# Kernel tuning notes

Measured on AMD Instinct MI355X. Metric: run time of the kernel, lower is better.

The kernel has to match this reference:

```python
import jax, jax.numpy as jnp
import numpy as np

BOUND = 25      # max decode steps
SOS = 1         # start-of-sequence token index
TEMP = 1.0      # temperature


def setup_inputs() -> dict:
    key = jax.random.key(0)
    ks = jax.random.split(key, 10)
    V, E, H, A, S = 50257, 1024, 1024, 1024, 2048
    return {
        "hidden": jax.random.normal(ks[0], (1, 1, H), dtype=jnp.float32),
        "embeddings": jax.random.normal(ks[1], (1, S, A), dtype=jnp.float32),
        "emb_table": jax.random.normal(ks[2], (V, E), dtype=jnp.float32) * 0.02,
        "W_ih": jax.random.normal(ks[3], (3 * H, E), dtype=jnp.float32) / np.sqrt(E).astype(np.float32),
        "W_hh": jax.random.normal(ks[4], (3 * H, H), dtype=jnp.float32) / np.sqrt(H).astype(np.float32),
        "b_ih": jnp.zeros((3 * H,), jnp.float32),
        "b_hh": jnp.zeros((3 * H,), jnp.float32),
        "W_e": jax.random.normal(ks[5], (A, A), dtype=jnp.float32) / np.sqrt(A).astype(np.float32),
        "W_q": jax.random.normal(ks[6], (A, H), dtype=jnp.float32) / np.sqrt(H).astype(np.float32),
        "b_a": jnp.zeros((A,), jnp.float32),
        "v_a": jax.random.normal(ks[7], (A,), dtype=jnp.float32) / np.sqrt(A).astype(np.float32),
        "W_out": jax.random.normal(ks[8], (V, H + A), dtype=jnp.float32) / np.sqrt(H + A).astype(np.float32),
        "b_out": jnp.zeros((V,), jnp.float32),
    }


def reference(hidden, embeddings, emb_table, W_ih, W_hh, b_ih, b_hh,
              W_e, W_q, b_a, v_a, W_out, b_out):
    """Greedy (top-1) autoregressive decode: per-step GRU + additive attention +
    vocab projection + softmax/argmax, for BOUND steps (EOS break replaced by
    fixed-length scan; faithful math per step, eval mode so dropout = identity).
    Returns (words [BOUND] int32, attention weights [1, BOUND, S])."""
    e = embeddings[0]                         # (S, A) encoder states
    eproj = e @ W_e.T + b_a                   # (S, A) precomputed key projection

    def step(carry, _):
        h, word = carry                       # h: (1, H), word: () int32
        x = emb_table[word][None, :]          # (1, E) input embedding
        # torch nn.GRU single-layer cell
        gi = x @ W_ih.T + b_ih                # (1, 3H)
        gh = h @ W_hh.T + b_hh                # (1, 3H)
        i_r, i_z, i_n = jnp.split(gi, 3, axis=-1)
        h_r, h_z, h_n = jnp.split(gh, 3, axis=-1)
        r = jax.nn.sigmoid(i_r + h_r)
        z = jax.nn.sigmoid(i_z + h_z)
        n = jnp.tanh(i_n + r * h_n)
        h = (1.0 - z) * n + z * h             # (1, H)
        # additive attention over encoder states (query broadcast over S)
        s = jnp.tanh(eproj + h @ W_q.T) @ v_a # (S,)
        w = jax.nn.softmax(s)                 # (S,) attention weights
        ctx = w @ e                           # (A,) context vector
        merge = jnp.concatenate([h[0], ctx])  # (H + A,) = cat([hidden[-1], attn])
        logits = (merge @ W_out.T + b_out) / TEMP   # (V,)
        word = jnp.argmax(logits).astype(jnp.int32) # top-1 sample
        return (h, word), (word, w)

    h0 = hidden[0]                            # last layer of encoder hidden (1, H)
    _, (words, weights) = jax.lax.scan(step, (h0, jnp.int32(SOS)), None, length=BOUND)
    return words, weights[None]               # (BOUND,), (1, BOUND, S)
```

## Files before the change

kernel.cpp:

```cpp
#include <hip/hip_runtime.h>
#include <cmath>

#define HSZ   1024
#define SSZ   2048
#define VSZ   50257
#define BOUND 25
#define SOS   1

__global__ __launch_bounds__(256) void init_kernel(const float* __restrict__ hidden,
                                                   float* __restrict__ h0,
                                                   int* __restrict__ wordp) {
    int i = blockIdx.x * 256 + threadIdx.x;
    if (i < HSZ) h0[i] = hidden[i];
    if (i == 0) *wordp = SOS;
}

#define BM 64
#define BN 64
#define BK 16
__global__ __launch_bounds__(256) void eproj_kernel(const float* __restrict__ e,
                                                    const float* __restrict__ We,
                                                    const float* __restrict__ b_a,
                                                    float* __restrict__ eproj) {
    __shared__ __align__(16) float As[BK][BM];
    __shared__ __align__(16) float Bs[BK][BN];
    const int tid = threadIdx.x;
    const int tx = tid & 15, ty = tid >> 4;
    const int arow0 = blockIdx.x * BM;
    const int brow0 = blockIdx.y * BN;
    const int lr = tid >> 2;
    const int lc = (tid & 3) * 4;

    float acc[4][4] = {};
    for (int k0 = 0; k0 < HSZ; k0 += BK) {
        float4 av = *(const float4*)&e [(size_t)(arow0 + lr) * HSZ + k0 + lc];
        float4 bv = *(const float4*)&We[(size_t)(brow0 + lr) * HSZ + k0 + lc];
        As[lc + 0][lr] = av.x; As[lc + 1][lr] = av.y;
        As[lc + 2][lr] = av.z; As[lc + 3][lr] = av.w;
        Bs[lc + 0][lr] = bv.x; Bs[lc + 1][lr] = bv.y;
        Bs[lc + 2][lr] = bv.z; Bs[lc + 3][lr] = bv.w;
        __syncthreads();
#pragma unroll
        for (int kk = 0; kk < BK; kk++) {
            float4 a4 = *(const float4*)&As[kk][ty * 4];
            float4 b4 = *(const float4*)&Bs[kk][tx * 4];
            float a[4] = {a4.x, a4.y, a4.z, a4.w};
            float b[4] = {b4.x, b4.y, b4.z, b4.w};
#pragma unroll
            for (int i = 0; i < 4; i++)
#pragma unroll
                for (int j = 0; j < 4; j++) acc[i][j] += a[i] * b[j];
        }
        __syncthreads();
    }
#pragma unroll
    for (int i = 0; i < 4; i++) {
        int s = arow0 + ty * 4 + i;
#pragma unroll
        for (int j = 0; j < 4; j++) {
            int a = brow0 + tx * 4 + j;
            eproj[(size_t)s * HSZ + a] = acc[i][j] + b_a[a];
        }
    }
}

__global__ __launch_bounds__(256) void gru_kernel(const float* __restrict__ emb_table,
                                                  const float* __restrict__ W_ih,
                                                  const float* __restrict__ W_hh,
                                                  const float* __restrict__ b_ih,
                                                  const float* __restrict__ b_hh,
                                                  const float* __restrict__ h_old,
                                                  const int* __restrict__ wordp,
                                                  float* __restrict__ h_new) {
    const int j = blockIdx.x;
    const int t = threadIdx.x;
    const int word = *wordp;
    const float* __restrict__ x = emb_table + (size_t)word * HSZ;

    float acc[6] = {0.f, 0.f, 0.f, 0.f, 0.f, 0.f};
    for (int c = t; c < HSZ; c += 256) {
        float xv = x[c], hv = h_old[c];
#pragma unroll
        for (int g = 0; g < 3; g++) {
            acc[g]     += W_ih[(size_t)(g * HSZ + j) * HSZ + c] * xv;
            acc[3 + g] += W_hh[(size_t)(g * HSZ + j) * HSZ + c] * hv;
        }
    }
    __shared__ float red[256];
    __shared__ float res[6];
    for (int g = 0; g < 6; g++) {
        red[t] = acc[g];
        __syncthreads();
        for (int s2 = 128; s2 > 0; s2 >>= 1) {
            if (t < s2) red[t] += red[t + s2];
            __syncthreads();
        }
        if (t == 0) res[g] = red[0];
        __syncthreads();
    }
    if (t == 0) {
        float ir = res[0] + b_ih[j];
        float iz = res[1] + b_ih[HSZ + j];
        float in_ = res[2] + b_ih[2 * HSZ + j];
        float hr = res[3] + b_hh[j];
        float hz = res[4] + b_hh[HSZ + j];
        float hn = res[5] + b_hh[2 * HSZ + j];
        float r = 1.f / (1.f + expf(-(ir + hr)));
        float z = 1.f / (1.f + expf(-(iz + hz)));
        float n = tanhf(in_ + r * hn);
        h_new[j] = (1.f - z) * n + z * h_old[j];
    }
}

__global__ __launch_bounds__(256) void q_kernel(const float* __restrict__ W_q,
                                                const float* __restrict__ h,
                                                float* __restrict__ q) {
    const int a = blockIdx.x, t = threadIdx.x;
    float acc = 0.f;
    for (int c = t; c < HSZ; c += 256) acc += W_q[(size_t)a * HSZ + c] * h[c];
    __shared__ float red[256];
    red[t] = acc;
    __syncthreads();
    for (int s2 = 128; s2 > 0; s2 >>= 1) {
        if (t < s2) red[t] += red[t + s2];
        __syncthreads();
    }
    if (t == 0) q[a] = red[0];
}

__global__ __launch_bounds__(256) void score_kernel(const float* __restrict__ eproj,
                                                    const float* __restrict__ q,
                                                    const float* __restrict__ v_a,
                                                    float* __restrict__ s) {
    const int k = blockIdx.x, t = threadIdx.x;
    float acc = 0.f;
    for (int c = t; c < HSZ; c += 256)
        acc += tanhf(eproj[(size_t)k * HSZ + c] + q[c]) * v_a[c];
    __shared__ float red[256];
    red[t] = acc;
    __syncthreads();
    for (int s2 = 128; s2 > 0; s2 >>= 1) {
        if (t < s2) red[t] += red[t + s2];
        __syncthreads();
    }
    if (t == 0) s[k] = red[0];
}

__global__ __launch_bounds__(256) void softmax_kernel(const float* __restrict__ s,
                                                      float* __restrict__ w,
                                                      float* __restrict__ ctx,
                                                      float* __restrict__ out_w) {
    const int t = threadIdx.x;
    __shared__ float red[256];
    float m = -INFINITY;
    for (int k = t; k < SSZ; k += 256) m = fmaxf(m, s[k]);
    red[t] = m;
    __syncthreads();
    for (int s2 = 128; s2 > 0; s2 >>= 1) {
        if (t < s2) red[t] = fmaxf(red[t], red[t + s2]);
        __syncthreads();
    }
    m = red[0];
    __syncthreads();
    float sum = 0.f;
    for (int k = t; k < SSZ; k += 256) {
        float ev = expf(s[k] - m);
        w[k] = ev;
        sum += ev;
    }
    red[t] = sum;
    __syncthreads();
    for (int s2 = 128; s2 > 0; s2 >>= 1) {
        if (t < s2) red[t] += red[t + s2];
        __syncthreads();
    }
    float inv = 1.f / red[0];
    for (int k = t; k < SSZ; k += 256) {
        float wv = w[k] * inv;
        w[k] = wv;
        out_w[k] = wv;
    }
    for (int c = t; c < HSZ; c += 256) ctx[c] = 0.f;
}

__global__ __launch_bounds__(256) void ctx_kernel(const float* __restrict__ e,
                                                  const float* __restrict__ w,
                                                  float* __restrict__ ctx) {
    const int a = blockIdx.y * 256 + threadIdx.x;
    const int k0 = blockIdx.x * 64;
    float acc = 0.f;
    for (int k = k0; k < k0 + 64; k++) acc += w[k] * e[(size_t)k * HSZ + a];
    atomicAdd(&ctx[a], acc);
}

__global__ __launch_bounds__(256) void logit_kernel(const float* __restrict__ W_out,
                                                    const float* __restrict__ b_out,
                                                    const float* __restrict__ h,
                                                    const float* __restrict__ ctx,
                                                    float* __restrict__ pval,
                                                    int* __restrict__ pidx) {
    __shared__ float merge[2 * HSZ];
    const int t = threadIdx.x;
    for (int c = t; c < HSZ; c += 256) {
        merge[c] = h[c];
        merge[HSZ + c] = ctx[c];
    }
    __syncthreads();
    const int wave = t >> 6, lane = t & 63;
    const int gw = blockIdx.x * 4 + wave;
    float best = -INFINITY;
    int bidx = 0x7fffffff;
    for (int v = gw; v < VSZ; v += 4096) {
        const float* __restrict__ row = W_out + (size_t)v * (2 * HSZ);
        float acc = 0.f;
#pragma unroll 8
        for (int c = lane; c < 2 * HSZ; c += 64) acc += row[c] * merge[c];
#pragma unroll
        for (int off = 32; off > 0; off >>= 1) acc += __shfl_down(acc, off, 64);
        if (lane == 0) {
            float logit = acc + b_out[v];
            if (logit > best) { best = logit; bidx = v; }
        }
    }
    __shared__ float bv[4];
    __shared__ int bi[4];
    if (lane == 0) { bv[wave] = best; bi[wave] = bidx; }
    __syncthreads();
    if (t == 0) {
        float B = bv[0]; int I = bi[0];
        for (int i = 1; i < 4; i++)
            if (bv[i] > B || (bv[i] == B && bi[i] < I)) { B = bv[i]; I = bi[i]; }
        pval[blockIdx.x] = B;
        pidx[blockIdx.x] = I;
    }
}

__global__ __launch_bounds__(256) void argmax_final_kernel(const float* __restrict__ pval,
                                                           const int* __restrict__ pidx,
                                                           int* __restrict__ wordp,
                                                           float* __restrict__ out_word) {
    const int t = threadIdx.x;
    float best = -INFINITY;
    int bidx = 0x7fffffff;
    for (int i = t; i < 1024; i += 256) {
        float v = pval[i];
        int id = pidx[i];
        if (v > best || (v == best && id < bidx)) { best = v; bidx = id; }
    }
    __shared__ float bv[256];
    __shared__ int bi[256];
    bv[t] = best; bi[t] = bidx;
    __syncthreads();
    for (int s2 = 128; s2 > 0; s2 >>= 1) {
        if (t < s2) {
            if (bv[t + s2] > bv[t] || (bv[t + s2] == bv[t] && bi[t + s2] < bi[t])) {
                bv[t] = bv[t + s2];
                bi[t] = bi[t + s2];
            }
        }
        __syncthreads();
    }
    if (t == 0) {
        *wordp = bi[0];
        *out_word = (float)bi[0];
    }
}

extern "C" void kernel_launch(void* const* d_in, const int* in_sizes, int n_in,
                              void* d_out, int out_size, void* d_ws, size_t ws_size,
                              hipStream_t stream) {
    const float* hidden     = (const float*)d_in[0];
    const float* embeddings = (const float*)d_in[1];
    const float* emb_table  = (const float*)d_in[2];
    const float* W_ih       = (const float*)d_in[3];
    const float* W_hh       = (const float*)d_in[4];
    const float* b_ih       = (const float*)d_in[5];
    const float* b_hh       = (const float*)d_in[6];
    const float* W_e        = (const float*)d_in[7];
    const float* W_q        = (const float*)d_in[8];
    const float* b_a        = (const float*)d_in[9];
    const float* v_a        = (const float*)d_in[10];
    const float* W_out      = (const float*)d_in[11];
    const float* b_out      = (const float*)d_in[12];

    float* out = (float*)d_out;
    float* ws  = (float*)d_ws;

    float* eproj = ws;
    float* h0    = ws + (size_t)SSZ * HSZ;
    float* h1    = h0 + HSZ;
    float* q     = h1 + HSZ;
    float* sc    = q + HSZ;
    float* w     = sc + SSZ;
    float* ctx   = w + SSZ;
    float* pval  = ctx + HSZ;
    int*   pidx  = (int*)(pval + 1024);
    int*   wordp = (int*)(pval + 2048);

    init_kernel<<<4, 256, 0, stream>>>(hidden, h0, wordp);
    dim3 egrid(SSZ / BM, HSZ / BN);
    eproj_kernel<<<egrid, 256, 0, stream>>>(embeddings, W_e, b_a, eproj);

    for (int t = 0; t < BOUND; t++) {
        float* hold = (t & 1) ? h1 : h0;
        float* hnew = (t & 1) ? h0 : h1;
        gru_kernel<<<HSZ, 256, 0, stream>>>(emb_table, W_ih, W_hh, b_ih, b_hh,
                                            hold, wordp, hnew);
        q_kernel<<<HSZ, 256, 0, stream>>>(W_q, hnew, q);
        score_kernel<<<SSZ, 256, 0, stream>>>(eproj, q, v_a, sc);
        softmax_kernel<<<1, 256, 0, stream>>>(sc, w, ctx, out + BOUND + (size_t)t * SSZ);
        ctx_kernel<<<dim3(32, 4), 256, 0, stream>>>(embeddings, w, ctx);
        logit_kernel<<<1024, 256, 0, stream>>>(W_out, b_out, hnew, ctx, pval, pidx);
        argmax_final_kernel<<<1, 256, 0, stream>>>(pval, pidx, wordp, out + t);
    }
}
```

Measured before the change: 3.326 ms.

## Fuse argmax into GRU, softmax into context kernel, vectorize matvecs with wave shuffles

```diff
diff --git a/kernel.cpp b/kernel.cpp
--- a/kernel.cpp
+++ b/kernel.cpp
@@ -6,13 +6,12 @@
 #define VSZ   50257
 #define BOUND 25
 #define SOS   1
+#define NPART 512
 
 __global__ __launch_bounds__(256) void init_kernel(const float* __restrict__ hidden,
-                                                   float* __restrict__ h0,
-                                                   int* __restrict__ wordp) {
+                                                   float* __restrict__ h0) {
     int i = blockIdx.x * 256 + threadIdx.x;
     if (i < HSZ) h0[i] = hidden[i];
-    if (i == 0) *wordp = SOS;
 }
 
 #define BM 64
@@ -70,35 +69,68 @@
                                                   const float* __restrict__ b_ih,
                                                   const float* __restrict__ b_hh,
                                                   const float* __restrict__ h_old,
-                                                  const int* __restrict__ wordp,
-                                                  float* __restrict__ h_new) {
+                                                  const float* __restrict__ pval,
+                                                  const int* __restrict__ pidx,
+                                                  int first,
+                                                  float* __restrict__ h_new,
+                                                  float* __restrict__ out_prev) {
+    const int t = threadIdx.x;
     const int j = blockIdx.x;
-    const int t = threadIdx.x;
-    const int word = *wordp;
+    __shared__ float rv[256];
+    __shared__ int ri[256];
+
+    int word;
+    if (!first) {
+        float bv = -INFINITY; int bi = 0x7fffffff;
+        for (int i = t; i < NPART; i += 256) {
+            float v = pval[i]; int id = pidx[i];
+            if (v > bv || (v == bv && id < bi)) { bv = v; bi = id; }
+        }
+        rv[t] = bv; ri[t] = bi;
+        __syncthreads();
+        for (int s2 = 128; s2 > 0; s2 >>= 1) {
+            if (t < s2) {
+                if (rv[t + s2] > rv[t] || (rv[t + s2] == rv[t] && ri[t + s2] < ri[t])) {
+                    rv[t] = rv[t + s2]; ri[t] = ri[t + s2];
+                }
+            }
+            __syncthreads();
+        }
+        word = ri[0];
+        if (j == 0 && t == 0 && out_prev) *out_prev = (float)word;
+    } else {
+        word = SOS;
+    }
+
     const float* __restrict__ x = emb_table + (size_t)word * HSZ;
-
-    float acc[6] = {0.f, 0.f, 0.f, 0.f, 0.f, 0.f};
-    for (int c = t; c < HSZ; c += 256) {
-        float xv = x[c], hv = h_old[c];
-#pragma unroll
-        for (int g = 0; g < 3; g++) {
-            acc[g]     += W_ih[(size_t)(g * HSZ + j) * HSZ + c] * xv;
-            acc[3 + g] += W_hh[(size_t)(g * HSZ + j) * HSZ + c] * hv;
-        }
-    }
-    __shared__ float red[256];
-    __shared__ float res[6];
-    for (int g = 0; g < 6; g++) {
-        red[t] = acc[g];
-        __syncthreads();
-        for (int s2 = 128; s2 > 0; s2 >>= 1) {
-            if (t < s2) red[t] += red[t + s2];
-            __syncthreads();
-        }
-        if (t == 0) res[g] = red[0];
-        __syncthreads();
-    }
+    const int c = t * 4;
+    float4 x4 = *(const float4*)&x[c];
+    float4 h4 = *(const float4*)&h_old[c];
+    float acc[6];
+#pragma unroll
+    for (int g = 0; g < 3; g++) {
+        float4 wi = *(const float4*)&W_ih[(size_t)(g * HSZ + j) * HSZ + c];
+        float4 wh = *(const float4*)&W_hh[(size_t)(g * HSZ + j) * HSZ + c];
+        acc[g]     = wi.x * x4.x + wi.y * x4.y + wi.z * x4.z + wi.w * x4.w;
+        acc[3 + g] = wh.x * h4.x + wh.y * h4.y + wh.z * h4.z + wh.w * h4.w;
+    }
+#pragma unroll
+    for (int g = 0; g < 6; g++)
+#pragma unroll
+        for (int off = 32; off > 0; off >>= 1) acc[g] += __shfl_down(acc[g], off, 64);
+
+    const int wave = t >> 6, lane = t & 63;
+    __shared__ float wred[4][6];
+    if (lane == 0) {
+#pragma unroll
+        for (int g = 0; g < 6; g++) wred[wave][g] = acc[g];
+    }
+    __syncthreads();
     if (t == 0) {
+        float res[6];
+#pragma unroll
+        for (int g = 0; g < 6; g++)
+            res[g] = wred[0][g] + wred[1][g] + wred[2][g] + wred[3][g];
         float ir = res[0] + b_ih[j];
         float iz = res[1] + b_ih[HSZ + j];
         float in_ = res[2] + b_ih[2 * HSZ + j];
@@ -116,42 +148,50 @@
                                                 const float* __restrict__ h,
                                                 float* __restrict__ q) {
     const int a = blockIdx.x, t = threadIdx.x;
-    float acc = 0.f;
-    for (int c = t; c < HSZ; c += 256) acc += W_q[(size_t)a * HSZ + c] * h[c];
-    __shared__ float red[256];
-    red[t] = acc;
-    __syncthreads();
-    for (int s2 = 128; s2 > 0; s2 >>= 1) {
-        if (t < s2) red[t] += red[t + s2];
-        __syncthreads();
-    }
-    if (t == 0) q[a] = red[0];
+    const int c = t * 4;
+    float4 wq = *(const float4*)&W_q[(size_t)a * HSZ + c];
+    float4 h4 = *(const float4*)&h[c];
+    float acc = wq.x * h4.x + wq.y * h4.y + wq.z * h4.z + wq.w * h4.w;
+#pragma unroll
+    for (int off = 32; off > 0; off >>= 1) acc += __shfl_down(acc, off, 64);
+    const int wave = t >> 6, lane = t & 63;
+    __shared__ float wred[4];
+    if (lane == 0) wred[wave] = acc;
+    __syncthreads();
+    if (t == 0) q[a] = wred[0] + wred[1] + wred[2] + wred[3];
 }
 
 __global__ __launch_bounds__(256) void score_kernel(const float* __restrict__ eproj,
                                                     const float* __restrict__ q,
                                                     const float* __restrict__ v_a,
-                                                    float* __restrict__ s) {
+                                                    float* __restrict__ s,
+                                                    float* __restrict__ ctx) {
     const int k = blockIdx.x, t = threadIdx.x;
-    float acc = 0.f;
-    for (int c = t; c < HSZ; c += 256)
-        acc += tanhf(eproj[(size_t)k * HSZ + c] + q[c]) * v_a[c];
+    if (k < 4) ctx[k * 256 + t] = 0.f;
+    const int c = t * 4;
+    float4 ev = *(const float4*)&eproj[(size_t)k * HSZ + c];
+    float4 q4 = *(const float4*)&q[c];
+    float4 v4 = *(const float4*)&v_a[c];
+    float acc = tanhf(ev.x + q4.x) * v4.x + tanhf(ev.y + q4.y) * v4.y +
+                tanhf(ev.z + q4.z) * v4.z + tanhf(ev.w + q4.w) * v4.w;
+#pragma unroll
+    for (int off = 32; off > 0; off >>= 1) acc += __shfl_down(acc, off, 64);
+    const int wave = t >> 6, lane = t & 63;
+    __shared__ float wred[4];
+    if (lane == 0) wred[wave] = acc;
+    __syncthreads();
+    if (t == 0) s[k] = wred[0] + wred[1] + wred[2] + wred[3];
+}
+
+__global__ __launch_bounds__(256) void attn_kernel(const float* __restrict__ s,
+                                                   const float* __restrict__ e,
+                                                   float* __restrict__ ctx,
+                                                   float* __restrict__ out_w) {
+    const int t = threadIdx.x;
+    const int kc = blockIdx.x;
+    const int ac = blockIdx.y;
     __shared__ float red[256];
-    red[t] = acc;
-    __syncthreads();
-    for (int s2 = 128; s2 > 0; s2 >>= 1) {
-        if (t < s2) red[t] += red[t + s2];
-        __syncthreads();
-    }
-    if (t == 0) s[k] = red[0];
-}
-
-__global__ __launch_bounds__(256) void softmax_kernel(const float* __restrict__ s,
-                                                      float* __restrict__ w,
-                                                      float* __restrict__ ctx,
-                                                      float* __restrict__ out_w) {
-    const int t = threadIdx.x;
-    __shared__ float red[256];
+
     float m = -INFINITY;
     for (int k = t; k < SSZ; k += 256) m = fmaxf(m, s[k]);
     red[t] = m;
@@ -162,12 +202,9 @@
     }
     m = red[0];
     __syncthreads();
+
     float sum = 0.f;
-    for (int k = t; k < SSZ; k += 256) {
-        float ev = expf(s[k] - m);
-        w[k] = ev;
-        sum += ev;
-    }
+    for (int k = t; k < SSZ; k += 256) sum += expf(s[k] - m);
     red[t] = sum;
     __syncthreads();
     for (int s2 = 128; s2 > 0; s2 >>= 1) {
@@ -175,21 +212,20 @@
         __syncthreads();
     }
     float inv = 1.f / red[0];
-    for (int k = t; k < SSZ; k += 256) {
-        float wv = w[k] * inv;
-        w[k] = wv;
-        out_w[k] = wv;
-    }
-    for (int c = t; c < HSZ; c += 256) ctx[c] = 0.f;
-}
-
-__global__ __launch_bounds__(256) void ctx_kernel(const float* __restrict__ e,
-                                                  const float* __restrict__ w,
-                                                  float* __restrict__ ctx) {
-    const int a = blockIdx.y * 256 + threadIdx.x;
-    const int k0 = blockIdx.x * 64;
+
+    __shared__ float wch[64];
+    if (t < 64) {
+        float wv = expf(s[kc * 64 + t] - m) * inv;
+        wch[t] = wv;
+        if (ac == 0) out_w[kc * 64 + t] = wv;
+    }
+    __syncthreads();
+
+    const int a = ac * 256 + t;
     float acc = 0.f;
-    for (int k = k0; k < k0 + 64; k++) acc += w[k] * e[(size_t)k * HSZ + a];
+#pragma unroll
+    for (int k = 0; k < 64; k++)
+        acc += wch[k] * e[(size_t)(kc * 64 + k) * HSZ + a];
     atomicAdd(&ctx[a], acc);
 }
 
@@ -199,22 +235,28 @@
                                                     const float* __restrict__ ctx,
                                                     float* __restrict__ pval,
                                                     int* __restrict__ pidx) {
-    __shared__ float merge[2 * HSZ];
+    __shared__ float4 mrg[512];
     const int t = threadIdx.x;
-    for (int c = t; c < HSZ; c += 256) {
-        merge[c] = h[c];
-        merge[HSZ + c] = ctx[c];
-    }
-    __syncthreads();
+    mrg[t]       = ((const float4*)h)[t];
+    mrg[256 + t] = ((const float4*)ctx)[t];
+    __syncthreads();
+
     const int wave = t >> 6, lane = t & 63;
+    float4 m[8];
+#pragma unroll
+    for (int i = 0; i < 8; i++) m[i] = mrg[lane + 64 * i];
+
     const int gw = blockIdx.x * 4 + wave;
     float best = -INFINITY;
     int bidx = 0x7fffffff;
-    for (int v = gw; v < VSZ; v += 4096) {
-        const float* __restrict__ row = W_out + (size_t)v * (2 * HSZ);
+    for (int v = gw; v < VSZ; v += 2048) {
+        const float4* __restrict__ row = (const float4*)(W_out + (size_t)v * (2 * HSZ));
         float acc = 0.f;
-#pragma unroll 8
-        for (int c = lane; c < 2 * HSZ; c += 64) acc += row[c] * merge[c];
+#pragma unroll
+        for (int i = 0; i < 8; i++) {
+            float4 r = row[lane + 64 * i];
+            acc += r.x * m[i].x + r.y * m[i].y + r.z * m[i].z + r.w * m[i].w;
+        }
 #pragma unroll
         for (int off = 32; off > 0; off >>= 1) acc += __shfl_down(acc, off, 64);
         if (lane == 0) {
@@ -235,35 +277,28 @@
     }
 }
 
-__global__ __launch_bounds__(256) void argmax_final_kernel(const float* __restrict__ pval,
-                                                           const int* __restrict__ pidx,
-                                                           int* __restrict__ wordp,
-                                                           float* __restrict__ out_word) {
+__global__ __launch_bounds__(256) void final_kernel(const float* __restrict__ pval,
+                                                    const int* __restrict__ pidx,
+                                                    float* __restrict__ out_word) {
     const int t = threadIdx.x;
-    float best = -INFINITY;
-    int bidx = 0x7fffffff;
-    for (int i = t; i < 1024; i += 256) {
-        float v = pval[i];
-        int id = pidx[i];
-        if (v > best || (v == best && id < bidx)) { best = v; bidx = id; }
-    }
-    __shared__ float bv[256];
-    __shared__ int bi[256];
-    bv[t] = best; bi[t] = bidx;
+    float bv = -INFINITY; int bi = 0x7fffffff;
+    for (int i = t; i < NPART; i += 256) {
+        float v = pval[i]; int id = pidx[i];
+        if (v > bv || (v == bv && id < bi)) { bv = v; bi = id; }
+    }
+    __shared__ float rv[256];
+    __shared__ int ri[256];
+    rv[t] = bv; ri[t] = bi;
     __syncthreads();
     for (int s2 = 128; s2 > 0; s2 >>= 1) {
         if (t < s2) {
-            if (bv[t + s2] > bv[t] || (bv[t + s2] == bv[t] && bi[t + s2] < bi[t])) {
-                bv[t] = bv[t + s2];
-                bi[t] = bi[t + s2];
+            if (rv[t + s2] > rv[t] || (rv[t + s2] == rv[t] && ri[t + s2] < ri[t])) {
+                rv[t] = rv[t + s2]; ri[t] = ri[t + s2];
             }
         }
         __syncthreads();
     }
-    if (t == 0) {
-        *wordp = bi[0];
-        *out_word = (float)bi[0];
-    }
+    if (t == 0) *out_word = (float)ri[0];
 }
 
 extern "C" void kernel_launch(void* const* d_in, const int* in_sizes, int n_in,
@@ -289,15 +324,13 @@
     float* eproj = ws;
     float* h0    = ws + (size_t)SSZ * HSZ;
     float* h1    = h0 + HSZ;
-    float* q     = h1 + HSZ;
-    float* sc    = q + HSZ;
-    float* w     = sc + SSZ;
-    float* ctx   = w + SSZ;
+    float* qv    = h1 + HSZ;
+    float* sc    = qv + HSZ;
+    float* ctx   = sc + SSZ;
     float* pval  = ctx + HSZ;
-    int*   pidx  = (int*)(pval + 1024);
-    int*   wordp = (int*)(pval + 2048);
-
-    init_kernel<<<4, 256, 0, stream>>>(hidden, h0, wordp);
+    int*   pidx  = (int*)(pval + NPART);
+
+    init_kernel<<<4, 256, 0, stream>>>(hidden, h0);
     dim3 egrid(SSZ / BM, HSZ / BN);
     eproj_kernel<<<egrid, 256, 0, stream>>>(embeddings, W_e, b_a, eproj);
 
@@ -305,12 +338,13 @@
         float* hold = (t & 1) ? h1 : h0;
         float* hnew = (t & 1) ? h0 : h1;
         gru_kernel<<<HSZ, 256, 0, stream>>>(emb_table, W_ih, W_hh, b_ih, b_hh,
-                                            hold, wordp, hnew);
-        q_kernel<<<HSZ, 256, 0, stream>>>(W_q, hnew, q);
-        score_kernel<<<SSZ, 256, 0, stream>>>(eproj, q, v_a, sc);
-        softmax_kernel<<<1, 256, 0, stream>>>(sc, w, ctx, out + BOUND + (size_t)t * SSZ);
-        ctx_kernel<<<dim3(32, 4), 256, 0, stream>>>(embeddings, w, ctx);
-        logit_kernel<<<1024, 256, 0, stream>>>(W_out, b_out, hnew, ctx, pval, pidx);
-        argmax_final_kernel<<<1, 256, 0, stream>>>(pval, pidx, wordp, out + t);
-    }
-}
+                                            hold, pval, pidx, (t == 0) ? 1 : 0,
+                                            hnew, (t > 0) ? out + (t - 1) : nullptr);
+        q_kernel<<<HSZ, 256, 0, stream>>>(W_q, hnew, qv);
+        score_kernel<<<SSZ, 256, 0, stream>>>(eproj, qv, v_a, sc, ctx);
+        attn_kernel<<<dim3(32, 4), 256, 0, stream>>>(sc, embeddings, ctx,
+                                                     out + BOUND + (size_t)t * SSZ);
+        logit_kernel<<<NPART, 256, 0, stream>>>(W_out, b_out, hnew, ctx, pval, pidx);
+    }
+    final_kernel<<<1, 256, 0, stream>>>(pval, pidx, out + (BOUND - 1));
+}
```

After: 4.034 ms. 1.21x slower.
